# Kernel optimization log

Hardware: AMD Instinct MI355X
Metric: run time of the kernel (lower is better)

Reference implementation:

```python
import jax, jax.numpy as jnp
import numpy as np

D_MODEL = 1024
HIDDEN = 64
N_STEPS = 6
T0, T1 = 0.0, 1.0


def setup_inputs() -> dict:
    key = jax.random.key(0)
    kx, k1, k2, k3, k4 = jax.random.split(key, 5)
    # PyTorch nn.Linear default init: U(-1/sqrt(fan_in), 1/sqrt(fan_in))
    s1 = 1.0 / np.sqrt(D_MODEL + 1)
    s2 = 1.0 / np.sqrt(HIDDEN)
    return {
        "x": jax.random.normal(kx, (8, 2048, D_MODEL), dtype=jnp.float32),
        "W1": jax.random.uniform(k1, (D_MODEL + 1, HIDDEN), jnp.float32, -s1, s1),
        "b1": jax.random.uniform(k2, (HIDDEN,), jnp.float32, -s1, s1),
        "W2": jax.random.uniform(k3, (HIDDEN, D_MODEL), jnp.float32, -s2, s2),
        "b2": jax.random.uniform(k4, (D_MODEL,), jnp.float32, -s2, s2),
    }


def _dynamics(t, z, W1, b1, W2, b2):
    # Equivalent to concat([z, t*ones], -1) @ W1: split the last row of W1
    # (the time channel) so we avoid materializing the concat.
    h = jnp.tanh(jnp.einsum("btd,dh->bth", z, W1[:-1]) + t * W1[-1] + b1)
    return jnp.einsum("bth,hd->btd", h, W2) + b2


def reference(x, W1, b1, W2, b2):
    h = (T1 - T0) / N_STEPS  # step size
    ts = T0 + h * jnp.arange(N_STEPS, dtype=x.dtype)

    def rk4_step(z, t):
        k1 = _dynamics(t, z, W1, b1, W2, b2)
        k2 = _dynamics(t + h / 2, z + (h / 2) * k1, W1, b1, W2, b2)
        k3 = _dynamics(t + h / 2, z + (h / 2) * k2, W1, b1, W2, b2)
        k4 = _dynamics(t + h, z + h * k3, W1, b1, W2, b2)
        z_next = z + (h / 6) * (k1 + 2 * k2 + 2 * k3 + k4)
        return z_next, None

    z_T, _ = jax.lax.scan(rk4_step, x, ts)
    return z_T
```

## Files before the change

kernel.cpp:

```cpp
#include <hip/hip_runtime.h>
#include <hip/hip_bf16.h>

#define DM 1024
#define HID 64
#define NSTEP 6
#define RSTEP (1.0f/6.0f)

using short8  = __attribute__((ext_vector_type(8))) short;
using short4v = __attribute__((ext_vector_type(4))) short;
using f32x4   = __attribute__((ext_vector_type(4))) float;

#define WS_W1P 0
#define WS_W2P 131072
#define WS_GP  262144
#define WS_U   270336
#define WS_VST 270592
#define WS_HU  276736

#define L_H0  0
#define L_H1  2304
#define L_HB  4608
#define L_VST 6912
#define L_HU  13056
#define L_B2  13312
#define LDS_TOTAL 17408
#define HP 144

#define BAR() asm volatile("s_waitcnt lgkmcnt(0)\n\ts_barrier" ::: "memory")

__device__ __forceinline__ short f2bf(float f) {
    __hip_bfloat16 h = __float2bfloat16(f);
    short s;
    __builtin_memcpy(&s, &h, 2);
    return s;
}
__device__ __forceinline__ float ftanh(float x) {
    x = fminf(fmaxf(x, -10.f), 10.f);
    float e = __expf(2.f * x);
    return __fdividef(e - 1.f, e + 1.f);
}

__global__ void k_prep(const float* __restrict__ W1, const float* __restrict__ W2,
                       const float* __restrict__ b1, const float* __restrict__ b2,
                       short* __restrict__ W1P, short* __restrict__ W2P,
                       short* __restrict__ GP, float* __restrict__ U,
                       float* __restrict__ VST, float* __restrict__ HU) {
    __shared__ float red[4][64];
    int b = blockIdx.x;
    int t = threadIdx.x;
    int l = t & 63, q4 = t >> 6;
    if (b < 32) {
        int kk = b, c = q4;
        int col = c * 16 + (l & 15);
        int kb = kk * 32 + ((l >> 4) << 3);
        short8 v;
        #pragma unroll
        for (int i = 0; i < 8; ++i) v[i] = f2bf(W1[(kb + i) * HID + col]);
        *(short8*)(W1P + (((kk * 4 + c) * 64) + l) * 8) = v;
    } else if (b < 64) {
        int unit = (b - 32) * 4 + q4;
        int kk2 = unit >> 6, ct = unit & 63;
        int col = ct * 16 + (l & 15);
        int kb = kk2 * 32 + ((l >> 4) << 3);
        short8 v;
        #pragma unroll
        for (int i = 0; i < 8; ++i) v[i] = f2bf(W2[(kb + i) * DM + col]);
        *(short8*)(W2P + (((kk2 * 64 + ct) * 64) + l) * 8) = v;
    } else if (b < 128) {
        int j = b - 64;
        float acc = 0.f;
        #pragma unroll 8
        for (int d = q4 * 256; d < q4 * 256 + 256; ++d)
            acc += W2[j * DM + d] * W1[d * HID + l];
        red[q4][l] = acc;
        __syncthreads();
        if (t < 64) {
            float a = red[0][l] + red[1][l] + red[2][l] + red[3][l];
            int kk = j >> 5, lk = (j >> 3) & 3, ii = j & 7, c = l >> 4, lo = l & 15;
            GP[(((kk * 4 + c) * 64) + lk * 16 + lo) * 8 + ii] = f2bf(a);
        }
    } else {
        float acc = 0.f;
        #pragma unroll 8
        for (int d = q4 * 256; d < q4 * 256 + 256; ++d)
            acc += b2[d] * W1[d * HID + l];
        red[q4][l] = acc;
        __syncthreads();
        if (t < 64) {
            float uu = red[0][l] + red[1][l] + red[2][l] + red[3][l];
            U[l] = uu;
            HU[l] = RSTEP * uu;
            float b1l = b1[l];
            float wtl = W1[DM * HID + l];
            #pragma unroll
            for (int s6 = 0; s6 < 6; ++s6) {
                float ts = RSTEP * (float)s6;
                float tm = ts + 0.5f * RSTEP;
                float vmid = b1l + tm * wtl + 0.5f * RSTEP * uu;
                VST[(s6 * 4 + 0) * 64 + l] = b1l + ts * wtl;
                VST[(s6 * 4 + 1) * 64 + l] = vmid;
                VST[(s6 * 4 + 2) * 64 + l] = vmid;
                VST[(s6 * 4 + 3) * 64 + l] = b1l + (ts + RSTEP) * wtl + RSTEP * uu;
            }
        }
    }
}

#define EPL(Wa,Wb,Wc,Wd,Xa,Xb,P) \
    Wa = w2p8[(P) * 64 + lane];        Wb = w2p8[((P) + 64) * 64 + lane]; \
    Wc = w2p8[((P) + 1) * 64 + lane];  Wd = w2p8[((P) + 65) * 64 + lane]; \
    Xa = *(const f32x4*)(xrow + (P) * 16 + (hq << 2)); \
    Xb = *(const f32x4*)(xrow + ((P) + 1) * 16 + (hq << 2));

#define EPC(Wa,Wb,Wc,Wd,Xa,Xb,P) { \
    f32x4 acc0 = (f32x4){0.f,0.f,0.f,0.f}, acc1 = (f32x4){0.f,0.f,0.f,0.f}; \
    acc0 = __builtin_amdgcn_mfma_f32_16x16x32_bf16(Wa, sb0, acc0, 0, 0, 0); \
    acc0 = __builtin_amdgcn_mfma_f32_16x16x32_bf16(Wb, sb1, acc0, 0, 0, 0); \
    acc1 = __builtin_amdgcn_mfma_f32_16x16x32_bf16(Wc, sb0, acc1, 0, 0, 0); \
    acc1 = __builtin_amdgcn_mfma_f32_16x16x32_bf16(Wd, sb1, acc1, 0, 0, 0); \
    f32x4 epc_bv0 = *(const f32x4*)(smem + L_B2 + ((P) * 16 + (hq << 2)) * 4); \
    f32x4 epc_bv1 = *(const f32x4*)(smem + L_B2 + (((P) + 1) * 16 + (hq << 2)) * 4); \
    f32x4 epc_n0, epc_n1; \
    for (int j = 0; j < 4; ++j) { epc_n0[j] = Xa[j] + acc0[j] + epc_bv0[j]; \
                                  epc_n1[j] = Xb[j] + acc1[j] + epc_bv1[j]; } \
    *(f32x4*)(orow + (P) * 16 + (hq << 2)) = epc_n0; \
    *(f32x4*)(orow + ((P) + 1) * 16 + (hq << 2)) = epc_n1; }

__global__ __launch_bounds__(256) __attribute__((amdgpu_waves_per_eu(2, 4)))
void k_ode(
        const float* __restrict__ X, const float* __restrict__ b2,
        const short* __restrict__ W1P, const short* __restrict__ W2P,
        const short* __restrict__ GP, const float* __restrict__ VST,
        const float* __restrict__ HU, float* __restrict__ OUT) {
    extern __shared__ char smem[];
    const int t = threadIdx.x;
    const int lane = t & 63;
    const int w = t >> 6;
    const int hq = lane >> 4;
    const int l15 = lane & 15;
    const int hcol0 = w * 16 + hq * 4;
    const size_t row0 = (size_t)blockIdx.x * 16;
    const float* xrow = X + (row0 + l15) * DM;

    *(f32x4*)(smem + L_B2 + t * 16) = *(const f32x4*)(b2 + t * 4);
    *(f32x4*)(smem + L_VST + t * 16) = *(const f32x4*)(VST + t * 4);
    if (t < 128)
        *(f32x4*)(smem + L_VST + 4096 + t * 16) = *(const f32x4*)(VST + 1024 + t * 4);
    else if (t < 144)
        *(f32x4*)(smem + L_HU + (t - 128) * 16) = *(const f32x4*)(HU + (t - 128) * 4);

    short8 gf0 = *(const short8*)(GP + (w * 64 + lane) * 8);
    short8 gf1 = *(const short8*)(GP + ((4 + w) * 64 + lane) * 8);

    f32x4 sz = (f32x4){0.f, 0.f, 0.f, 0.f};
    {
        const short8* wp = (const short8*)W1P;
        #pragma unroll
        for (int B = 0; B < 4; ++B) {
            f32x4 lo[8], hi[8];
            #pragma unroll
            for (int i = 0; i < 8; ++i) {
                const float* xp = xrow + ((B * 8 + i) << 5) + (hq << 3);
                lo[i] = *(const f32x4*)(xp);
                hi[i] = *(const f32x4*)(xp + 4);
            }
            #pragma unroll
            for (int i = 0; i < 8; ++i) {
                int kk = B * 8 + i;
                short8 zf;
                #pragma unroll
                for (int j = 0; j < 4; ++j) { zf[j] = f2bf(lo[i][j]); zf[4 + j] = f2bf(hi[i][j]); }
                sz = __builtin_amdgcn_mfma_f32_16x16x32_bf16(
                         wp[(kk * 4 + w) * 64 + lane], zf, sz, 0, 0, 0);
            }
        }
    }
    BAR();

    f32x4 ssum = (f32x4){0.f, 0.f, 0.f, 0.f};

    for (int s = 0; s < NSTEP; ++s) {
        f32x4 hsum;

        {
            f32x4 vst = *(const f32x4*)(smem + L_VST + (s * 4 + 0) * 256 + hcol0 * 4);
            short4v hc;
            #pragma unroll
            for (int j = 0; j < 4; ++j) {
                float h = ftanh(sz[j] + vst[j]);
                hsum[j] = h;
                hc[j] = f2bf(h);
            }
            *(short4v*)(smem + L_H0 + l15 * HP + hcol0 * 2) = hc;
        }
        BAR();

        #pragma unroll
        for (int e = 1; e < 4; ++e) {
            const float ce = (e == 3) ? RSTEP : (0.5f * RSTEP);
            const float we = (e == 3) ? 1.f : 2.f;
            const int rbuf = (e == 2) ? L_H1 : L_H0;
            const int wbuf = (e == 1) ? L_H1 : ((e == 2) ? L_H0 : L_HB);

            short8 hf0 = *(const short8*)(smem + rbuf + l15 * HP + (hq << 4));
            short8 hf1 = *(const short8*)(smem + rbuf + l15 * HP + 64 + (hq << 4));
            f32x4 dd = (f32x4){0.f, 0.f, 0.f, 0.f};
            dd = __builtin_amdgcn_mfma_f32_16x16x32_bf16(gf0, hf0, dd, 0, 0, 0);
            dd = __builtin_amdgcn_mfma_f32_16x16x32_bf16(gf1, hf1, dd, 0, 0, 0);
            f32x4 vst = *(const f32x4*)(smem + L_VST + (s * 4 + e) * 256 + hcol0 * 4);
            short4v hc;
            #pragma unroll
            for (int j = 0; j < 4; ++j) {
                float h = ftanh(sz[j] + ce * dd[j] + vst[j]);
                hsum[j] += we * h;
                if (e < 3) {
                    hc[j] = f2bf(h);
                } else {
                    ssum[j] += hsum[j] * (RSTEP / 6.f);
                    hc[j] = (s < NSTEP - 1) ? f2bf(hsum[j] * (RSTEP / 6.f))
                                            : f2bf(ssum[j]);
                }
            }
            *(short4v*)(smem + wbuf + l15 * HP + hcol0 * 2) = hc;
            BAR();
        }

        if (s < NSTEP - 1) {
            short8 hb0 = *(const short8*)(smem + L_HB + l15 * HP + (hq << 4));
            short8 hb1 = *(const short8*)(smem + L_HB + l15 * HP + 64 + (hq << 4));
            f32x4 d = (f32x4){0.f, 0.f, 0.f, 0.f};
            d = __builtin_amdgcn_mfma_f32_16x16x32_bf16(gf0, hb0, d, 0, 0, 0);
            d = __builtin_amdgcn_mfma_f32_16x16x32_bf16(gf1, hb1, d, 0, 0, 0);
            f32x4 hu4 = *(const f32x4*)(smem + L_HU + hcol0 * 4);
            #pragma unroll
            for (int j = 0; j < 4; ++j)
                sz[j] += d[j] + hu4[j];
        }
    }

    {
        short8 sb0 = *(const short8*)(smem + L_HB + l15 * HP + (hq << 4));
        short8 sb1 = *(const short8*)(smem + L_HB + l15 * HP + 64 + (hq << 4));
        const short8* w2p8 = (const short8*)W2P;
        float* orow = OUT + (row0 + l15) * DM;
        const int ctbase = w * 16;

        short8 wA0, wA1, wA2, wA3; f32x4 xA0, xA1;
        short8 wB0, wB1, wB2, wB3; f32x4 xB0, xB1;
        EPL(wA0, wA1, wA2, wA3, xA0, xA1, ctbase)
        #pragma unroll
        for (int p = 0; p < 16; p += 4) {
            EPL(wB0, wB1, wB2, wB3, xB0, xB1, ctbase + p + 2)
            EPC(wA0, wA1, wA2, wA3, xA0, xA1, ctbase + p)
            if (p + 4 < 16) { EPL(wA0, wA1, wA2, wA3, xA0, xA1, ctbase + p + 4) }
            EPC(wB0, wB1, wB2, wB3, xB0, xB1, ctbase + p + 2)
        }
    }
}

extern "C" void kernel_launch(void* const* d_in, const int* in_sizes, int n_in,
                              void* d_out, int out_size, void* d_ws, size_t ws_size,
                              hipStream_t stream) {
    (void)in_sizes; (void)n_in; (void)out_size; (void)ws_size;
    const float* X  = (const float*)d_in[0];
    const float* W1 = (const float*)d_in[1];
    const float* b1 = (const float*)d_in[2];
    const float* W2 = (const float*)d_in[3];
    const float* b2 = (const float*)d_in[4];
    float* OUT = (float*)d_out;
    short* W1P = (short*)((char*)d_ws + WS_W1P);
    short* W2P = (short*)((char*)d_ws + WS_W2P);
    short* GP  = (short*)((char*)d_ws + WS_GP);
    float* U   = (float*)((char*)d_ws + WS_U);
    float* VST = (float*)((char*)d_ws + WS_VST);
    float* HU  = (float*)((char*)d_ws + WS_HU);

    k_prep<<<129, 256, 0, stream>>>(W1, W2, b1, b2, W1P, W2P, GP, U, VST, HU);
    k_ode<<<1024, 256, LDS_TOTAL, stream>>>(X, b2, W1P, W2P, GP, VST, HU, OUT);
}
```

Measured before the change: 77.45 us.

## Process two 16-row tiles per block to share weights and barriers

Each block now handles 32 rows as two independent 16-row tiles (A and B). Weight fragments for W1, the G matrix and W2 are loaded once and reused for both tiles, and each barrier in the RK4 loop now covers twice the work. The grid is halved to 512 blocks and LDS grows to hold a second set of hidden buffers. The tradeoff is more registers and fewer blocks, which cuts available parallelism on a 256-CU device.

```diff
diff --git a/kernel.cpp b/kernel.cpp
--- a/kernel.cpp
+++ b/kernel.cpp
@@ -17,13 +17,16 @@
 #define WS_VST 270592
 #define WS_HU  276736
 
-#define L_H0  0
-#define L_H1  2304
-#define L_HB  4608
-#define L_VST 6912
-#define L_HU  13056
-#define L_B2  13312
-#define LDS_TOTAL 17408
+#define L_H0A  0
+#define L_H1A  2304
+#define L_HBA  4608
+#define L_H0B  6912
+#define L_H1B  9216
+#define L_HBB  11520
+#define L_VST  13824
+#define L_HU   19968
+#define L_B2   20224
+#define LDS_TOTAL 24320
 #define HP 144
 
 #define BAR() asm volatile("s_waitcnt lgkmcnt(0)\n\ts_barrier" ::: "memory")
@@ -106,25 +109,36 @@
     }
 }
 
-#define EPL(Wa,Wb,Wc,Wd,Xa,Xb,P) \
+#define EPL2(Wa,Wb,Wc,Wd,P) \
     Wa = w2p8[(P) * 64 + lane];        Wb = w2p8[((P) + 64) * 64 + lane]; \
-    Wc = w2p8[((P) + 1) * 64 + lane];  Wd = w2p8[((P) + 65) * 64 + lane]; \
-    Xa = *(const f32x4*)(xrow + (P) * 16 + (hq << 2)); \
-    Xb = *(const f32x4*)(xrow + ((P) + 1) * 16 + (hq << 2));
-
-#define EPC(Wa,Wb,Wc,Wd,Xa,Xb,P) { \
-    f32x4 acc0 = (f32x4){0.f,0.f,0.f,0.f}, acc1 = (f32x4){0.f,0.f,0.f,0.f}; \
-    acc0 = __builtin_amdgcn_mfma_f32_16x16x32_bf16(Wa, sb0, acc0, 0, 0, 0); \
-    acc0 = __builtin_amdgcn_mfma_f32_16x16x32_bf16(Wb, sb1, acc0, 0, 0, 0); \
-    acc1 = __builtin_amdgcn_mfma_f32_16x16x32_bf16(Wc, sb0, acc1, 0, 0, 0); \
-    acc1 = __builtin_amdgcn_mfma_f32_16x16x32_bf16(Wd, sb1, acc1, 0, 0, 0); \
+    Wc = w2p8[((P) + 1) * 64 + lane];  Wd = w2p8[((P) + 65) * 64 + lane];
+
+#define EPC2(Wa,Wb,Wc,Wd,P) { \
+    f32x4 epc_xa0 = *(const f32x4*)(xrowA + (P) * 16 + (hq << 2)); \
+    f32x4 epc_xa1 = *(const f32x4*)(xrowA + ((P) + 1) * 16 + (hq << 2)); \
+    f32x4 epc_xb0 = *(const f32x4*)(xrowB + (P) * 16 + (hq << 2)); \
+    f32x4 epc_xb1 = *(const f32x4*)(xrowB + ((P) + 1) * 16 + (hq << 2)); \
+    f32x4 accA0 = (f32x4){0.f,0.f,0.f,0.f}, accA1 = accA0, accB0 = accA0, accB1 = accA0; \
+    accA0 = __builtin_amdgcn_mfma_f32_16x16x32_bf16(Wa, sbA0, accA0, 0, 0, 0); \
+    accA0 = __builtin_amdgcn_mfma_f32_16x16x32_bf16(Wb, sbA1, accA0, 0, 0, 0); \
+    accA1 = __builtin_amdgcn_mfma_f32_16x16x32_bf16(Wc, sbA0, accA1, 0, 0, 0); \
+    accA1 = __builtin_amdgcn_mfma_f32_16x16x32_bf16(Wd, sbA1, accA1, 0, 0, 0); \
+    accB0 = __builtin_amdgcn_mfma_f32_16x16x32_bf16(Wa, sbB0, accB0, 0, 0, 0); \
+    accB0 = __builtin_amdgcn_mfma_f32_16x16x32_bf16(Wb, sbB1, accB0, 0, 0, 0); \
+    accB1 = __builtin_amdgcn_mfma_f32_16x16x32_bf16(Wc, sbB0, accB1, 0, 0, 0); \
+    accB1 = __builtin_amdgcn_mfma_f32_16x16x32_bf16(Wd, sbB1, accB1, 0, 0, 0); \
     f32x4 epc_bv0 = *(const f32x4*)(smem + L_B2 + ((P) * 16 + (hq << 2)) * 4); \
     f32x4 epc_bv1 = *(const f32x4*)(smem + L_B2 + (((P) + 1) * 16 + (hq << 2)) * 4); \
-    f32x4 epc_n0, epc_n1; \
-    for (int j = 0; j < 4; ++j) { epc_n0[j] = Xa[j] + acc0[j] + epc_bv0[j]; \
-                                  epc_n1[j] = Xb[j] + acc1[j] + epc_bv1[j]; } \
-    *(f32x4*)(orow + (P) * 16 + (hq << 2)) = epc_n0; \
-    *(f32x4*)(orow + ((P) + 1) * 16 + (hq << 2)) = epc_n1; }
+    f32x4 epc_nA0, epc_nA1, epc_nB0, epc_nB1; \
+    for (int j = 0; j < 4; ++j) { \
+        epc_nA0[j] = epc_xa0[j] + accA0[j] + epc_bv0[j]; \
+        epc_nA1[j] = epc_xa1[j] + accA1[j] + epc_bv1[j]; \
+        epc_nB0[j] = epc_xb0[j] + accB0[j] + epc_bv0[j]; \
+        epc_nB1[j] = epc_xb1[j] + accB1[j] + epc_bv1[j]; } \
+    *(f32x4*)(orowA + (P) * 16 + (hq << 2)) = epc_nA0; \
+    *(f32x4*)(orowA + ((P) + 1) * 16 + (hq << 2)) = epc_nA1; \
+    *(f32x4*)(orowB + (P) * 16 + (hq << 2)) = epc_nB0; \
+    *(f32x4*)(orowB + ((P) + 1) * 16 + (hq << 2)) = epc_nB1; }
 
 __global__ __launch_bounds__(256) __attribute__((amdgpu_waves_per_eu(2, 4)))
 void k_ode(
@@ -139,8 +153,9 @@
     const int hq = lane >> 4;
     const int l15 = lane & 15;
     const int hcol0 = w * 16 + hq * 4;
-    const size_t row0 = (size_t)blockIdx.x * 16;
-    const float* xrow = X + (row0 + l15) * DM;
+    const size_t row0 = (size_t)blockIdx.x * 32;
+    const float* xrowA = X + (row0 + l15) * DM;
+    const float* xrowB = X + (row0 + 16 + l15) * DM;
 
     *(f32x4*)(smem + L_B2 + t * 16) = *(const f32x4*)(b2 + t * 4);
     *(f32x4*)(smem + L_VST + t * 16) = *(const f32x4*)(VST + t * 4);
@@ -152,46 +167,60 @@
     short8 gf0 = *(const short8*)(GP + (w * 64 + lane) * 8);
     short8 gf1 = *(const short8*)(GP + ((4 + w) * 64 + lane) * 8);
 
-    f32x4 sz = (f32x4){0.f, 0.f, 0.f, 0.f};
+    f32x4 szA = (f32x4){0.f, 0.f, 0.f, 0.f};
+    f32x4 szB = (f32x4){0.f, 0.f, 0.f, 0.f};
     {
         const short8* wp = (const short8*)W1P;
         #pragma unroll
-        for (int B = 0; B < 4; ++B) {
-            f32x4 lo[8], hi[8];
-            #pragma unroll
-            for (int i = 0; i < 8; ++i) {
-                const float* xp = xrow + ((B * 8 + i) << 5) + (hq << 3);
-                lo[i] = *(const f32x4*)(xp);
-                hi[i] = *(const f32x4*)(xp + 4);
-            }
-            #pragma unroll
-            for (int i = 0; i < 8; ++i) {
-                int kk = B * 8 + i;
-                short8 zf;
+        for (int Bb = 0; Bb < 8; ++Bb) {
+            f32x4 loA[4], hiA[4], loB[4], hiB[4];
+            #pragma unroll
+            for (int i = 0; i < 4; ++i) {
+                const float* xp = xrowA + ((Bb * 4 + i) << 5) + (hq << 3);
+                loA[i] = *(const f32x4*)(xp);
+                hiA[i] = *(const f32x4*)(xp + 4);
+            }
+            #pragma unroll
+            for (int i = 0; i < 4; ++i) {
+                const float* xp = xrowB + ((Bb * 4 + i) << 5) + (hq << 3);
+                loB[i] = *(const f32x4*)(xp);
+                hiB[i] = *(const f32x4*)(xp + 4);
+            }
+            #pragma unroll
+            for (int i = 0; i < 4; ++i) {
+                int kk = Bb * 4 + i;
+                short8 zfA, zfB;
                 #pragma unroll
-                for (int j = 0; j < 4; ++j) { zf[j] = f2bf(lo[i][j]); zf[4 + j] = f2bf(hi[i][j]); }
-                sz = __builtin_amdgcn_mfma_f32_16x16x32_bf16(
-                         wp[(kk * 4 + w) * 64 + lane], zf, sz, 0, 0, 0);
+                for (int j = 0; j < 4; ++j) {
+                    zfA[j] = f2bf(loA[i][j]); zfA[4 + j] = f2bf(hiA[i][j]);
+                    zfB[j] = f2bf(loB[i][j]); zfB[4 + j] = f2bf(hiB[i][j]);
+                }
+                short8 wf = wp[(kk * 4 + w) * 64 + lane];
+                szA = __builtin_amdgcn_mfma_f32_16x16x32_bf16(wf, zfA, szA, 0, 0, 0);
+                szB = __builtin_amdgcn_mfma_f32_16x16x32_bf16(wf, zfB, szB, 0, 0, 0);
             }
         }
     }
     BAR();
 
-    f32x4 ssum = (f32x4){0.f, 0.f, 0.f, 0.f};
+    f32x4 ssumA = (f32x4){0.f, 0.f, 0.f, 0.f};
+    f32x4 ssumB = (f32x4){0.f, 0.f, 0.f, 0.f};
 
     for (int s = 0; s < NSTEP; ++s) {
-        f32x4 hsum;
+        f32x4 hsumA, hsumB;
 
         {
             f32x4 vst = *(const f32x4*)(smem + L_VST + (s * 4 + 0) * 256 + hcol0 * 4);
-            short4v hc;
+            short4v hcA, hcB;
             #pragma unroll
             for (int j = 0; j < 4; ++j) {
-                float h = ftanh(sz[j] + vst[j]);
-                hsum[j] = h;
-                hc[j] = f2bf(h);
-            }
-            *(short4v*)(smem + L_H0 + l15 * HP + hcol0 * 2) = hc;
+                float hA = ftanh(szA[j] + vst[j]);
+                float hB = ftanh(szB[j] + vst[j]);
+                hsumA[j] = hA; hsumB[j] = hB;
+                hcA[j] = f2bf(hA); hcB[j] = f2bf(hB);
+            }
+            *(short4v*)(smem + L_H0A + l15 * HP + hcol0 * 2) = hcA;
+            *(short4v*)(smem + L_H0B + l15 * HP + hcol0 * 2) = hcB;
         }
         BAR();
 
@@ -199,61 +228,81 @@
         for (int e = 1; e < 4; ++e) {
             const float ce = (e == 3) ? RSTEP : (0.5f * RSTEP);
             const float we = (e == 3) ? 1.f : 2.f;
-            const int rbuf = (e == 2) ? L_H1 : L_H0;
-            const int wbuf = (e == 1) ? L_H1 : ((e == 2) ? L_H0 : L_HB);
-
-            short8 hf0 = *(const short8*)(smem + rbuf + l15 * HP + (hq << 4));
-            short8 hf1 = *(const short8*)(smem + rbuf + l15 * HP + 64 + (hq << 4));
-            f32x4 dd = (f32x4){0.f, 0.f, 0.f, 0.f};
-            dd = __builtin_amdgcn_mfma_f32_16x16x32_bf16(gf0, hf0, dd, 0, 0, 0);
-            dd = __builtin_amdgcn_mfma_f32_16x16x32_bf16(gf1, hf1, dd, 0, 0, 0);
+            const int rbA = (e == 2) ? L_H1A : L_H0A;
+            const int wbA = (e == 1) ? L_H1A : ((e == 2) ? L_H0A : L_HBA);
+            const int rbB = (e == 2) ? L_H1B : L_H0B;
+            const int wbB = (e == 1) ? L_H1B : ((e == 2) ? L_H0B : L_HBB);
+
+            short8 hfA0 = *(const short8*)(smem + rbA + l15 * HP + (hq << 4));
+            short8 hfA1 = *(const short8*)(smem + rbA + l15 * HP + 64 + (hq << 4));
+            short8 hfB0 = *(const short8*)(smem + rbB + l15 * HP + (hq << 4));
+            short8 hfB1 = *(const short8*)(smem + rbB + l15 * HP + 64 + (hq << 4));
+            f32x4 ddA = (f32x4){0.f, 0.f, 0.f, 0.f};
+            f32x4 ddB = (f32x4){0.f, 0.f, 0.f, 0.f};
+            ddA = __builtin_amdgcn_mfma_f32_16x16x32_bf16(gf0, hfA0, ddA, 0, 0, 0);
+            ddB = __builtin_amdgcn_mfma_f32_16x16x32_bf16(gf0, hfB0, ddB, 0, 0, 0);
+            ddA = __builtin_amdgcn_mfma_f32_16x16x32_bf16(gf1, hfA1, ddA, 0, 0, 0);
+            ddB = __builtin_amdgcn_mfma_f32_16x16x32_bf16(gf1, hfB1, ddB, 0, 0, 0);
             f32x4 vst = *(const f32x4*)(smem + L_VST + (s * 4 + e) * 256 + hcol0 * 4);
-            short4v hc;
+            short4v hcA, hcB;
             #pragma unroll
             for (int j = 0; j < 4; ++j) {
-                float h = ftanh(sz[j] + ce * dd[j] + vst[j]);
-                hsum[j] += we * h;
+                float hA = ftanh(szA[j] + ce * ddA[j] + vst[j]);
+                float hB = ftanh(szB[j] + ce * ddB[j] + vst[j]);
+                hsumA[j] += we * hA; hsumB[j] += we * hB;
                 if (e < 3) {
-                    hc[j] = f2bf(h);
+                    hcA[j] = f2bf(hA); hcB[j] = f2bf(hB);
                 } else {
-                    ssum[j] += hsum[j] * (RSTEP / 6.f);
-                    hc[j] = (s < NSTEP - 1) ? f2bf(hsum[j] * (RSTEP / 6.f))
-                                            : f2bf(ssum[j]);
+                    ssumA[j] += hsumA[j] * (RSTEP / 6.f);
+                    ssumB[j] += hsumB[j] * (RSTEP / 6.f);
+                    hcA[j] = (s < NSTEP - 1) ? f2bf(hsumA[j] * (RSTEP / 6.f)) : f2bf(ssumA[j]);
+                    hcB[j] = (s < NSTEP - 1) ? f2bf(hsumB[j] * (RSTEP / 6.f)) : f2bf(ssumB[j]);
                 }
             }
-            *(short4v*)(smem + wbuf + l15 * HP + hcol0 * 2) = hc;
+            *(short4v*)(smem + wbA + l15 * HP + hcol0 * 2) = hcA;
+            *(short4v*)(smem + wbB + l15 * HP + hcol0 * 2) = hcB;
             BAR();
         }
 
         if (s < NSTEP - 1) {
-            short8 hb0 = *(const short8*)(smem + L_HB + l15 * HP + (hq << 4));
-            short8 hb1 = *(const short8*)(smem + L_HB + l15 * HP + 64 + (hq << 4));
-            f32x4 d = (f32x4){0.f, 0.f, 0.f, 0.f};
-            d = __builtin_amdgcn_mfma_f32_16x16x32_bf16(gf0, hb0, d, 0, 0, 0);
-            d = __builtin_amdgcn_mfma_f32_16x16x32_bf16(gf1, hb1, d, 0, 0, 0);
+            short8 hbA0 = *(const short8*)(smem + L_HBA + l15 * HP + (hq << 4));
+            short8 hbA1 = *(const short8*)(smem + L_HBA + l15 * HP + 64 + (hq << 4));
+            short8 hbB0 = *(const short8*)(smem + L_HBB + l15 * HP + (hq << 4));
+            short8 hbB1 = *(const short8*)(smem + L_HBB + l15 * HP + 64 + (hq << 4));
+            f32x4 dA = (f32x4){0.f, 0.f, 0.f, 0.f};
+            f32x4 dB = (f32x4){0.f, 0.f, 0.f, 0.f};
+            dA = __builtin_amdgcn_mfma_f32_16x16x32_bf16(gf0, hbA0, dA, 0, 0, 0);
+            dB = __builtin_amdgcn_mfma_f32_16x16x32_bf16(gf0, hbB0, dB, 0, 0, 0);
+            dA = __builtin_amdgcn_mfma_f32_16x16x32_bf16(gf1, hbA1, dA, 0, 0, 0);
+            dB = __builtin_amdgcn_mfma_f32_16x16x32_bf16(gf1, hbB1, dB, 0, 0, 0);
             f32x4 hu4 = *(const f32x4*)(smem + L_HU + hcol0 * 4);
             #pragma unroll
-            for (int j = 0; j < 4; ++j)
-                sz[j] += d[j] + hu4[j];
+            for (int j = 0; j < 4; ++j) {
+                szA[j] += dA[j] + hu4[j];
+                szB[j] += dB[j] + hu4[j];
+            }
         }
     }
 
     {
-        short8 sb0 = *(const short8*)(smem + L_HB + l15 * HP + (hq << 4));
-        short8 sb1 = *(const short8*)(smem + L_HB + l15 * HP + 64 + (hq << 4));
+        short8 sbA0 = *(const short8*)(smem + L_HBA + l15 * HP + (hq << 4));
+        short8 sbA1 = *(const short8*)(smem + L_HBA + l15 * HP + 64 + (hq << 4));
+        short8 sbB0 = *(const short8*)(smem + L_HBB + l15 * HP + (hq << 4));
+        short8 sbB1 = *(const short8*)(smem + L_HBB + l15 * HP + 64 + (hq << 4));
         const short8* w2p8 = (const short8*)W2P;
-        float* orow = OUT + (row0 + l15) * DM;
+        float* orowA = OUT + (row0 + l15) * DM;
+        float* orowB = OUT + (row0 + 16 + l15) * DM;
         const int ctbase = w * 16;
 
-        short8 wA0, wA1, wA2, wA3; f32x4 xA0, xA1;
-        short8 wB0, wB1, wB2, wB3; f32x4 xB0, xB1;
-        EPL(wA0, wA1, wA2, wA3, xA0, xA1, ctbase)
+        short8 wA0, wA1, wA2, wA3;
+        short8 wB0, wB1, wB2, wB3;
+        EPL2(wA0, wA1, wA2, wA3, ctbase)
         #pragma unroll
         for (int p = 0; p < 16; p += 4) {
-            EPL(wB0, wB1, wB2, wB3, xB0, xB1, ctbase + p + 2)
-            EPC(wA0, wA1, wA2, wA3, xA0, xA1, ctbase + p)
-            if (p + 4 < 16) { EPL(wA0, wA1, wA2, wA3, xA0, xA1, ctbase + p + 4) }
-            EPC(wB0, wB1, wB2, wB3, xB0, xB1, ctbase + p + 2)
+            EPL2(wB0, wB1, wB2, wB3, ctbase + p + 2)
+            EPC2(wA0, wA1, wA2, wA3, ctbase + p)
+            if (p + 4 < 16) { EPL2(wA0, wA1, wA2, wA3, ctbase + p + 4) }
+            EPC2(wB0, wB1, wB2, wB3, ctbase + p + 2)
         }
     }
 }
@@ -276,5 +325,5 @@
     float* HU  = (float*)((char*)d_ws + WS_HU);
 
     k_prep<<<129, 256, 0, stream>>>(W1, W2, b1, b2, W1P, W2P, GP, U, VST, HU);
-    k_ode<<<1024, 256, LDS_TOTAL, stream>>>(X, b2, W1P, W2P, GP, VST, HU, OUT);
-}
+    k_ode<<<512, 256, LDS_TOTAL, stream>>>(X, b2, W1P, W2P, GP, VST, HU, OUT);
+}
```

After: 76.81 us. About the same (-0.8%).
